# Optimization experiments

Measured on AMD Instinct MI355X. Metric: run time of the kernel, lower is better.

## Reference

```python
import jax, jax.numpy as jnp
import numpy as np

GROUPS = 8
NUM_HEADS = 4
EPS = 1e-5

def setup_inputs() -> dict:
    key = jax.random.key(0)
    k1, k2, k3 = jax.random.split(key, 3)
    B, C, H, W = 4, 128, 64, 64
    x = jax.random.normal(k1, (B, C, H, W), dtype=jnp.float32)
    gn_w = jnp.ones((C,), jnp.float32)
    gn_b = jnp.zeros((C,), jnp.float32)
    qkv_w = jax.random.normal(k2, (3 * C, C), dtype=jnp.float32) * (1.0 / np.sqrt(C))
    qkv_b = jnp.zeros((3 * C,), jnp.float32)
    proj_w = jax.random.normal(k3, (C, C), dtype=jnp.float32) * (1.0 / np.sqrt(C))
    proj_b = jnp.zeros((C,), jnp.float32)
    return {"x": x, "gn_w": gn_w, "gn_b": gn_b, "qkv_w": qkv_w,
            "qkv_b": qkv_b, "proj_w": proj_w, "proj_b": proj_b}

def group_norm(x, w, b):
    B, C, H, W = x.shape
    xg = x.reshape(B, GROUPS, C // GROUPS, H, W)
    mean = jnp.mean(xg, axis=(2, 3, 4), keepdims=True)
    var = jnp.var(xg, axis=(2, 3, 4), keepdims=True)
    xn = ((xg - mean) * jax.lax.rsqrt(var + EPS)).reshape(B, C, H, W)
    return xn * w[None, :, None, None] + b[None, :, None, None]

def reference(x, gn_w, gn_b, qkv_w, qkv_b, proj_w, proj_b):
    B, C, H, W = x.shape
    nh = NUM_HEADS
    hd = C // nh
    xn = group_norm(x, gn_w, gn_b)  # residual is the NORMALIZED x (torch code reassigns x)
    # 1x1 conv == channel matmul
    qkv = jnp.einsum('oc,bchw->bohw', qkv_w, xn) + qkv_b[None, :, None, None]
    qkv = qkv.reshape(B, 3, nh, hd, H * W)
    q, k, v = qkv[:, 0], qkv[:, 1], qkv[:, 2]          # [B, nh, hd, HW]
    attn = jnp.einsum('bhcd,bhce->bhde', q, k) * (C ** -0.5)  # note: full-C scale, as in torch code
    attn = jax.nn.softmax(attn, axis=-1)
    out = jnp.einsum('bhde,bhce->bhcd', attn, v).reshape(B, C, H, W)
    out = jnp.einsum('oc,bchw->bohw', proj_w, out) + proj_b[None, :, None, None]
    return out + xn
```

## Files before the change

### kernel.cpp

```cpp
#include <hip/hip_runtime.h>
#include <math.h>

#define BATCH 4
#define C 128
#define HW 4096
#define G 8
#define CPG 16
#define NH 4
#define HD 32
#define EPS 1e-5f
#define SCALE 0.08838834764831845f
#define LOG2E 1.44269504088896340f
#define KP 40
#define GP 136

typedef unsigned int uint;
typedef unsigned short ushort;
typedef __attribute__((ext_vector_type(8))) short bf16x8;
typedef __attribute__((ext_vector_type(4))) float f32x4;

__device__ __forceinline__ ushort f2bf(float x) {
  uint u = __float_as_uint(x);
  u += 0x7fff + ((u >> 16) & 1);
  return (ushort)(u >> 16);
}
__device__ __forceinline__ ushort f2bf_r(float x) {
  return (ushort)((__float_as_uint(x) + 0x8000u) >> 16);
}
__device__ __forceinline__ float bf2f(ushort h) {
  return __uint_as_float(((uint)h) << 16);
}
__device__ __forceinline__ uint pk(float a, float b) {
#if __has_builtin(__builtin_amdgcn_cvt_pk_bf16_f32)
  auto r = __builtin_amdgcn_cvt_pk_bf16_f32(a, b);
  union { decltype(r) v; uint u; } x;
  x.v = r;
  return x.u;
#else
  uint ua = __float_as_uint(a) + 0x8000u;
  uint ub = __float_as_uint(b) + 0x8000u;
  return __builtin_amdgcn_perm(ub, ua, 0x07060302);
#endif
}
__device__ __forceinline__ bf16x8 as_bf(uint4 u) {
  union { uint4 a; bf16x8 b; } x; x.a = u; return x.b;
}
__device__ __forceinline__ float fexp2(float x) {
#if __has_builtin(__builtin_amdgcn_exp2f)
  return __builtin_amdgcn_exp2f(x);
#else
  return __exp2f(x);
#endif
}

__global__ __launch_bounds__(256) void gn_part(
    const float* __restrict__ x, float* __restrict__ stats) {
  const int bg = blockIdx.x >> 3, chunk = blockIdx.x & 7;
  const float* xp = x + (size_t)bg * (CPG * HW) + chunk * 8192;
  const int tid = threadIdx.x;
  float s = 0.f, ss = 0.f;
  #pragma unroll
  for (int j = 0; j < 8; j++) {
    float4 v = ((const float4*)xp)[j * 256 + tid];
    s += (v.x + v.y) + (v.z + v.w);
    ss += (v.x * v.x + v.y * v.y) + (v.z * v.z + v.w * v.w);
  }
  #pragma unroll
  for (int off = 32; off; off >>= 1) {
    s  += __shfl_down(s, off);
    ss += __shfl_down(ss, off);
  }
  __shared__ float rs[4], rss[4];
  const int lane = tid & 63, wid = tid >> 6;
  if (lane == 0) { rs[wid] = s; rss[wid] = ss; }
  __syncthreads();
  if (tid == 0) {
    stats[(bg * 8 + chunk) * 2]     = (rs[0] + rs[1]) + (rs[2] + rs[3]);
    stats[(bg * 8 + chunk) * 2 + 1] = (rss[0] + rss[1]) + (rss[2] + rss[3]);
  }
}

__device__ __forceinline__ void gn_coeff(
    const float* __restrict__ stats, const float* __restrict__ w,
    const float* __restrict__ b, int batch, int c, float& ca, float& cb) {
  const int bg = batch * G + (c >> 4);
  float s = 0.f, ss = 0.f;
  #pragma unroll
  for (int k = 0; k < 8; k++) {
    s  += stats[(bg * 8 + k) * 2];
    ss += stats[(bg * 8 + k) * 2 + 1];
  }
  const float mean = s * (1.0f / 65536.0f);
  const float var  = ss * (1.0f / 65536.0f) - mean * mean;
  const float inv  = rsqrtf(var + EPS);
  ca = w[c] * inv;
  cb = b[c] - mean * ca;
}

__global__ __launch_bounds__(256) void qkv_gemm(
    const float* __restrict__ x, const float* __restrict__ stats,
    const float* __restrict__ gnw, const float* __restrict__ gnb,
    const float* __restrict__ w, const float* __restrict__ bias,
    ushort* __restrict__ qkvb) {
  const int b = blockIdx.z, m0 = blockIdx.y * 64, n0 = blockIdx.x * 64;
  const int tid = threadIdx.x, lane = tid & 63, wv = tid >> 6;
  const int li = lane & 15, g = lane >> 4;
  __shared__ ushort Ws[64][GP];
  __shared__ ushort Xs[64][GP];
  __shared__ float CA[C], CB[C];

  if (tid < C) gn_coeff(stats, gnw, gnb, b, tid, CA[tid], CB[tid]);
  __syncthreads();

  {
    const int row = tid >> 2, c0 = (tid & 3) * 32;
    const float* wr = w + (size_t)(m0 + row) * C + c0;
    #pragma unroll
    for (int k = 0; k < 4; k++) {
      float4 f0 = ((const float4*)wr)[k * 2];
      float4 f1 = ((const float4*)wr)[k * 2 + 1];
      uint4 u = {pk(f0.x, f0.y), pk(f0.z, f0.w), pk(f1.x, f1.y), pk(f1.z, f1.w)};
      *(uint4*)&Ws[row][c0 + k * 8] = u;
    }
  }
  {
    const int nX = tid & 63, c0 = (tid >> 6) * 32;
    const float* xb = x + (size_t)(b * C + c0) * HW + n0 + nX;
    #pragma unroll
    for (int k = 0; k < 4; k++) {
      float xv[8];
      #pragma unroll
      for (int j = 0; j < 8; j++) {
        int c = c0 + k * 8 + j;
        xv[j] = fmaf(xb[(size_t)(k * 8 + j) * HW], CA[c], CB[c]);
      }
      uint4 u = {pk(xv[0], xv[1]), pk(xv[2], xv[3]), pk(xv[4], xv[5]), pk(xv[6], xv[7])};
      *(uint4*)&Xs[nX][c0 + k * 8] = u;
    }
  }
  __syncthreads();

  f32x4 acc[4];
  #pragma unroll
  for (int nt = 0; nt < 4; nt++) acc[nt] = (f32x4){0.f, 0.f, 0.f, 0.f};
  #pragma unroll
  for (int kk = 0; kk < 4; kk++) {
    bf16x8 af = *(const bf16x8*)&Ws[wv * 16 + li][kk * 32 + g * 8];
    #pragma unroll
    for (int nt = 0; nt < 4; nt++) {
      bf16x8 bfr = *(const bf16x8*)&Xs[nt * 16 + li][kk * 32 + g * 8];
      acc[nt] = __builtin_amdgcn_mfma_f32_16x16x32_bf16(af, bfr, acc[nt], 0, 0, 0);
    }
  }
  const int ob = m0 + wv * 16 + g * 4;
  #pragma unroll
  for (int r = 0; r < 4; r++) {
    float bi = bias[ob + r];
    #pragma unroll
    for (int nt = 0; nt < 4; nt++) {
      qkvb[(size_t)(b * 3 * C + ob + r) * HW + n0 + nt * 16 + li] = f2bf(acc[nt][r] + bi);
    }
  }
}

__global__ __launch_bounds__(256) void kvprep_kernel(
    const ushort* __restrict__ qkvb, ushort* __restrict__ kt) {
  const int bh = blockIdx.y, b = bh >> 2, h = bh & 3;
  const int e0 = blockIdx.x * 64;
  const ushort* kp = qkvb + (size_t)(b * 3 * C + C + h * HD) * HW;
  ushort* ktp = kt + (size_t)bh * HW * HD;
  const int t = threadIdx.x;

  __shared__ ushort Kt[32][66];
  {
    const int c = t >> 3, e8 = (t & 7) * 8;
    *(uint4*)&Kt[c][e8] = *(const uint4*)&kp[(size_t)c * HW + e0 + e8];
  }
  __syncthreads();
  {
    const int e = t >> 2, c0 = (t & 3) * 8;
    ushort o[8];
    #pragma unroll
    for (int j = 0; j < 8; j++) o[j] = Kt[c0 + j][e];
    uint4 u;
    u.x = o[0] | ((uint)o[1] << 16);
    u.y = o[2] | ((uint)o[3] << 16);
    u.z = o[4] | ((uint)o[5] << 16);
    u.w = o[6] | ((uint)o[7] << 16);
    *(uint4*)&ktp[(size_t)(e0 + e) * HD + c0] = u;
  }
}

__global__ __launch_bounds__(512, 4) void attn_kernel(
    ushort* __restrict__ qkv, const ushort* __restrict__ kt) {
  const int bh = blockIdx.y, b = bh >> 2, h = bh & 3;
  const int tid = threadIdx.x, lane = tid & 63, wv = tid >> 6;
  const int li = lane & 15, g = lane >> 4;
  const int grp = wv >> 2, w4 = wv & 3;
  ushort* qp = qkv + (size_t)(b * 3 * C + h * HD) * HW;
  const ushort* vpl = qkv + (size_t)(b * 3 * C + 2 * C + h * HD) * HW;
  const ushort* ktp = kt + (size_t)bh * HW * HD;
  const int d0 = blockIdx.x * 128 + w4 * 32;

  struct SmemT {
    union {
      struct { ushort Ks[2][2][32][KP]; ushort Vs[2][2][32][KP]; } t;
      float OP[8][64][19];
    };
  };
  __shared__ SmemT sm;

  const float qs = SCALE * LOG2E;
  bf16x8 qf[2];
  #pragma unroll
  for (int dt = 0; dt < 2; dt++) {
    int d = d0 + dt * 16 + li;
    float qv[8];
    #pragma unroll
    for (int j = 0; j < 8; j++)
      qv[j] = bf2f(qp[(size_t)(g * 8 + j) * HW + d]) * qs;
    uint4 qu = {pk(qv[0], qv[1]), pk(qv[2], qv[3]), pk(qv[4], qv[5]), pk(qv[6], qv[7])};
    qf[dt] = as_bf(qu);
  }

  f32x4 O[2][2];
  #pragma unroll
  for (int dt = 0; dt < 2; dt++)
    #pragma unroll
    for (int ct = 0; ct < 2; ct++) O[dt][ct] = (f32x4){0.f, 0.f, 0.f, 0.f};
  f32x4 lacc[2] = {(f32x4){0.f, 0.f, 0.f, 0.f}, (f32x4){0.f, 0.f, 0.f, 0.f}};
  const uint one2 = 0x3F803F80u;
  const bf16x8 ones = as_bf((uint4){one2, one2, one2, one2});

  const int gt = tid & 255;
  const bool isK = gt < 128;
  const int t2 = gt & 127;
  const int srow = t2 >> 2, scol8 = (t2 & 3) * 8;
  const ushort* gK = ktp + (size_t)(grp * 64) * 1024 + t2 * 8;
  const ushort* gV = vpl + (size_t)srow * HW + grp * 2048 + scol8;

  uint4 st = isK ? *(const uint4*)&gK[0] : *(const uint4*)&gV[0];
  if (isK) *(uint4*)&sm.t.Ks[grp][0][srow][scol8] = st;
  else     *(uint4*)&sm.t.Vs[grp][0][srow][scol8] = st;
  st = isK ? *(const uint4*)&gK[1024] : *(const uint4*)&gV[32];
  __syncthreads();

  for (int it = 0; it < 64; it++) {
    const int cur = it & 1, nxt = cur ^ 1;
    if (isK) *(uint4*)&sm.t.Ks[grp][nxt][srow][scol8] = st;
    else     *(uint4*)&sm.t.Vs[grp][nxt][srow][scol8] = st;

    bf16x8 kf0 = *(const bf16x8*)&sm.t.Ks[grp][cur][li][g * 8];
    bf16x8 kf1 = *(const bf16x8*)&sm.t.Ks[grp][cur][16 + li][g * 8];
    uint2 va0 = *(const uint2*)&sm.t.Vs[grp][cur][li][4 * g];
    uint2 va1 = *(const uint2*)&sm.t.Vs[grp][cur][li][16 + 4 * g];
    uint2 vb0 = *(const uint2*)&sm.t.Vs[grp][cur][16 + li][4 * g];
    uint2 vb1 = *(const uint2*)&sm.t.Vs[grp][cur][16 + li][16 + 4 * g];
    bf16x8 vf0 = as_bf((uint4){va0.x, va0.y, va1.x, va1.y});
    bf16x8 vf1 = as_bf((uint4){vb0.x, vb0.y, vb1.x, vb1.y});

    const int tn = (it + 2) & 63;
    st = isK ? *(const uint4*)&gK[(size_t)tn * 1024] : *(const uint4*)&gV[tn * 32];

    const f32x4 z = (f32x4){0.f, 0.f, 0.f, 0.f};
    #pragma unroll
    for (int dt = 0; dt < 2; dt++) {
      f32x4 s0 = __builtin_amdgcn_mfma_f32_16x16x32_bf16(kf0, qf[dt], z, 0, 0, 0);
      f32x4 s1 = __builtin_amdgcn_mfma_f32_16x16x32_bf16(kf1, qf[dt], z, 0, 0, 0);
      float p0 = fexp2(s0[0]), p1 = fexp2(s0[1]), p2 = fexp2(s0[2]), p3 = fexp2(s0[3]);
      float p4 = fexp2(s1[0]), p5 = fexp2(s1[1]), p6 = fexp2(s1[2]), p7 = fexp2(s1[3]);
      uint4 pu = {pk(p0, p1), pk(p2, p3), pk(p4, p5), pk(p6, p7)};
      bf16x8 pf = as_bf(pu);
      lacc[dt] = __builtin_amdgcn_mfma_f32_16x16x32_bf16(ones, pf, lacc[dt], 0, 0, 0);
      O[dt][0] = __builtin_amdgcn_mfma_f32_16x16x32_bf16(vf0, pf, O[dt][0], 0, 0, 0);
      O[dt][1] = __builtin_amdgcn_mfma_f32_16x16x32_bf16(vf1, pf, O[dt][1], 0, 0, 0);
    }
    __syncthreads();
  }

  #pragma unroll
  for (int dt = 0; dt < 2; dt++) {
    #pragma unroll
    for (int ct = 0; ct < 2; ct++)
      #pragma unroll
      for (int r = 0; r < 4; r++) sm.OP[wv][lane][dt * 8 + ct * 4 + r] = O[dt][ct][r];
    sm.OP[wv][lane][16 + dt] = lacc[dt][0];
  }
  __syncthreads();
  const int pw = wv ^ 4;
  #pragma unroll
  for (int dt = 0; dt < 2; dt++) {
    const float inv = 1.0f / (lacc[dt][0] + sm.OP[pw][lane][16 + dt]);
    const int d = d0 + dt * 16 + li;
    #pragma unroll
    for (int r = 0; r < 4; r++) {
      float val = O[dt][grp][r] + sm.OP[pw][lane][dt * 8 + grp * 4 + r];
      qp[(size_t)(grp * 16 + g * 4 + r) * HW + d] = f2bf_r(val * inv);
    }
  }
}

__global__ __launch_bounds__(256) void proj_gemm(
    const ushort* __restrict__ qkvb, const float* __restrict__ w,
    const float* __restrict__ bias, const float* __restrict__ x,
    const float* __restrict__ stats, const float* __restrict__ gnw,
    const float* __restrict__ gnb, float* __restrict__ out) {
  const int b = blockIdx.z, m0 = blockIdx.y * 64, n0 = blockIdx.x * 64;
  const int tid = threadIdx.x, lane = tid & 63, wv = tid >> 6;
  const int li = lane & 15, g = lane >> 4;
  __shared__ ushort Ws[64][GP];
  __shared__ ushort Xs[64][GP];
  __shared__ float CA[64], CB[64];

  if (tid < 64) gn_coeff(stats, gnw, gnb, b, m0 + tid, CA[tid], CB[tid]);

  {
    const int row = tid >> 2, c0 = (tid & 3) * 32;
    const float* wr = w + (size_t)(m0 + row) * C + c0;
    #pragma unroll
    for (int k = 0; k < 4; k++) {
      float4 f0 = ((const float4*)wr)[k * 2];
      float4 f1 = ((const float4*)wr)[k * 2 + 1];
      uint4 u = {pk(f0.x, f0.y), pk(f0.z, f0.w), pk(f1.x, f1.y), pk(f1.z, f1.w)};
      *(uint4*)&Ws[row][c0 + k * 8] = u;
    }
  }
  {
    const int nX = tid & 63, c0 = (tid >> 6) * 32;
    const ushort* xb = qkvb + (size_t)(b * 3 * C + c0) * HW + n0 + nX;
    #pragma unroll
    for (int k = 0; k < 4; k++) {
      ushort t8[8];
      #pragma unroll
      for (int j = 0; j < 8; j++) t8[j] = xb[(size_t)(k * 8 + j) * HW];
      uint4 u;
      u.x = t8[0] | ((uint)t8[1] << 16);
      u.y = t8[2] | ((uint)t8[3] << 16);
      u.z = t8[4] | ((uint)t8[5] << 16);
      u.w = t8[6] | ((uint)t8[7] << 16);
      *(uint4*)&Xs[nX][c0 + k * 8] = u;
    }
  }
  __syncthreads();

  f32x4 acc[4];
  #pragma unroll
  for (int nt = 0; nt < 4; nt++) acc[nt] = (f32x4){0.f, 0.f, 0.f, 0.f};
  #pragma unroll
  for (int kk = 0; kk < 4; kk++) {
    bf16x8 af = *(const bf16x8*)&Ws[wv * 16 + li][kk * 32 + g * 8];
    #pragma unroll
    for (int nt = 0; nt < 4; nt++) {
      bf16x8 bfr = *(const bf16x8*)&Xs[nt * 16 + li][kk * 32 + g * 8];
      acc[nt] = __builtin_amdgcn_mfma_f32_16x16x32_bf16(af, bfr, acc[nt], 0, 0, 0);
    }
  }
  const int ob = m0 + wv * 16 + g * 4;
  #pragma unroll
  for (int r = 0; r < 4; r++) {
    const float bi = bias[ob + r];
    const float ca = CA[wv * 16 + g * 4 + r], cb = CB[wv * 16 + g * 4 + r];
    #pragma unroll
    for (int nt = 0; nt < 4; nt++) {
      size_t idx = (size_t)(b * C + ob + r) * HW + n0 + nt * 16 + li;
      out[idx] = acc[nt][r] + bi + fmaf(x[idx], ca, cb);
    }
  }
}

extern "C" void kernel_launch(void* const* d_in, const int* in_sizes, int n_in,
                              void* d_out, int out_size, void* d_ws, size_t ws_size,
                              hipStream_t stream) {
  const float* x     = (const float*)d_in[0];
  const float* gn_w  = (const float*)d_in[1];
  const float* gn_b  = (const float*)d_in[2];
  const float* qkv_w = (const float*)d_in[3];
  const float* qkv_b = (const float*)d_in[4];
  const float* pw    = (const float*)d_in[5];
  const float* pb    = (const float*)d_in[6];
  float* out = (float*)d_out;

  float*  stats = (float*)d_ws;
  ushort* qkvb  = (ushort*)((char*)d_ws + 4096);
  ushort* kt    = qkvb + (size_t)BATCH * 3 * C * HW;

  gn_part<<<dim3(256), dim3(256), 0, stream>>>(x, stats);
  qkv_gemm<<<dim3(HW / 64, 6, BATCH), dim3(256), 0, stream>>>(
      x, stats, gn_w, gn_b, qkv_w, qkv_b, qkvb);
  kvprep_kernel<<<dim3(HW / 64, BATCH * NH), dim3(256), 0, stream>>>(qkvb, kt);
  attn_kernel<<<dim3(HW / 128, BATCH * NH), dim3(512), 0, stream>>>(qkvb, kt);
  proj_gemm<<<dim3(HW / 64, 2, BATCH), dim3(256), 0, stream>>>(
      qkvb, pw, pb, x, stats, gn_w, gn_b, out);
}
```

Measured before the change: 162.1 us.

## Fuse K transpose into QKV GEMM epilogue and drop kvprep kernel

The QKV GEMM now writes the K block straight into the transposed [e][HD] layout used by attention, so the separate kvprep transpose kernel and its extra read/write pass over K are gone. The attention kernel's shared-memory union of K/V tiles and the output-reduction buffer is also split into separate arrays. The K epilogue now does scattered 2-byte stores with a stride of HD, which coalesces poorly. The attention kernel's larger shared-memory footprint (~59KB vs ~39KB) may reduce occupancy under launch_bounds(512,4).

```diff
diff --git a/kernel.cpp b/kernel.cpp
--- a/kernel.cpp
+++ b/kernel.cpp
@@ -11,7 +11,6 @@
 #define EPS 1e-5f
 #define SCALE 0.08838834764831845f
 #define LOG2E 1.44269504088896340f
-#define KP 40
 #define GP 136
 
 typedef unsigned int uint;
@@ -101,7 +100,7 @@
     const float* __restrict__ x, const float* __restrict__ stats,
     const float* __restrict__ gnw, const float* __restrict__ gnb,
     const float* __restrict__ w, const float* __restrict__ bias,
-    ushort* __restrict__ qkvb) {
+    ushort* __restrict__ qkvb, ushort* __restrict__ kt) {
   const int b = blockIdx.z, m0 = blockIdx.y * 64, n0 = blockIdx.x * 64;
   const int tid = threadIdx.x, lane = tid & 63, wv = tid >> 6;
   const int li = lane & 15, g = lane >> 4;
@@ -153,41 +152,29 @@
     }
   }
   const int ob = m0 + wv * 16 + g * 4;
-  #pragma unroll
-  for (int r = 0; r < 4; r++) {
-    float bi = bias[ob + r];
-    #pragma unroll
-    for (int nt = 0; nt < 4; nt++) {
-      qkvb[(size_t)(b * 3 * C + ob + r) * HW + n0 + nt * 16 + li] = f2bf(acc[nt][r] + bi);
-    }
-  }
-}
-
-__global__ __launch_bounds__(256) void kvprep_kernel(
-    const ushort* __restrict__ qkvb, ushort* __restrict__ kt) {
-  const int bh = blockIdx.y, b = bh >> 2, h = bh & 3;
-  const int e0 = blockIdx.x * 64;
-  const ushort* kp = qkvb + (size_t)(b * 3 * C + C + h * HD) * HW;
-  ushort* ktp = kt + (size_t)bh * HW * HD;
-  const int t = threadIdx.x;
-
-  __shared__ ushort Kt[32][66];
-  {
-    const int c = t >> 3, e8 = (t & 7) * 8;
-    *(uint4*)&Kt[c][e8] = *(const uint4*)&kp[(size_t)c * HW + e0 + e8];
-  }
-  __syncthreads();
-  {
-    const int e = t >> 2, c0 = (t & 3) * 8;
-    ushort o[8];
-    #pragma unroll
-    for (int j = 0; j < 8; j++) o[j] = Kt[c0 + j][e];
-    uint4 u;
-    u.x = o[0] | ((uint)o[1] << 16);
-    u.y = o[2] | ((uint)o[3] << 16);
-    u.z = o[4] | ((uint)o[5] << 16);
-    u.w = o[6] | ((uint)o[7] << 16);
-    *(uint4*)&ktp[(size_t)(e0 + e) * HD + c0] = u;
+  if (blockIdx.y == 2 || blockIdx.y == 3) {
+    const int ck = ob - C;
+    const int h  = ck >> 5;
+    const int cl = ck & 31;
+    ushort* ktp = kt + (size_t)(b * NH + h) * HW * HD;
+    #pragma unroll
+    for (int r = 0; r < 4; r++) {
+      float bi = bias[ob + r];
+      #pragma unroll
+      for (int nt = 0; nt < 4; nt++) {
+        int e = n0 + nt * 16 + li;
+        ktp[(size_t)e * HD + cl + r] = f2bf(acc[nt][r] + bi);
+      }
+    }
+  } else {
+    #pragma unroll
+    for (int r = 0; r < 4; r++) {
+      float bi = bias[ob + r];
+      #pragma unroll
+      for (int nt = 0; nt < 4; nt++) {
+        qkvb[(size_t)(b * 3 * C + ob + r) * HW + n0 + nt * 16 + li] = f2bf(acc[nt][r] + bi);
+      }
+    }
   }
 }
 
@@ -202,13 +189,9 @@
   const ushort* ktp = kt + (size_t)bh * HW * HD;
   const int d0 = blockIdx.x * 128 + w4 * 32;
 
-  struct SmemT {
-    union {
-      struct { ushort Ks[2][2][32][KP]; ushort Vs[2][2][32][KP]; } t;
-      float OP[8][64][19];
-    };
-  };
-  __shared__ SmemT sm;
+  __shared__ ushort Ks[2][2][32][40];
+  __shared__ ushort Vs[2][2][32][40];
+  __shared__ float OP[8][64][19];
 
   const float qs = SCALE * LOG2E;
   bf16x8 qf[2];
@@ -240,22 +223,22 @@
   const ushort* gV = vpl + (size_t)srow * HW + grp * 2048 + scol8;
 
   uint4 st = isK ? *(const uint4*)&gK[0] : *(const uint4*)&gV[0];
-  if (isK) *(uint4*)&sm.t.Ks[grp][0][srow][scol8] = st;
-  else     *(uint4*)&sm.t.Vs[grp][0][srow][scol8] = st;
+  if (isK) *(uint4*)&Ks[grp][0][srow][scol8] = st;
+  else     *(uint4*)&Vs[grp][0][srow][scol8] = st;
   st = isK ? *(const uint4*)&gK[1024] : *(const uint4*)&gV[32];
   __syncthreads();
 
   for (int it = 0; it < 64; it++) {
     const int cur = it & 1, nxt = cur ^ 1;
-    if (isK) *(uint4*)&sm.t.Ks[grp][nxt][srow][scol8] = st;
-    else     *(uint4*)&sm.t.Vs[grp][nxt][srow][scol8] = st;
-
-    bf16x8 kf0 = *(const bf16x8*)&sm.t.Ks[grp][cur][li][g * 8];
-    bf16x8 kf1 = *(const bf16x8*)&sm.t.Ks[grp][cur][16 + li][g * 8];
-    uint2 va0 = *(const uint2*)&sm.t.Vs[grp][cur][li][4 * g];
-    uint2 va1 = *(const uint2*)&sm.t.Vs[grp][cur][li][16 + 4 * g];
-    uint2 vb0 = *(const uint2*)&sm.t.Vs[grp][cur][16 + li][4 * g];
-    uint2 vb1 = *(const uint2*)&sm.t.Vs[grp][cur][16 + li][16 + 4 * g];
+    if (isK) *(uint4*)&Ks[grp][nxt][srow][scol8] = st;
+    else     *(uint4*)&Vs[grp][nxt][srow][scol8] = st;
+
+    bf16x8 kf0 = *(const bf16x8*)&Ks[grp][cur][li][g * 8];
+    bf16x8 kf1 = *(const bf16x8*)&Ks[grp][cur][16 + li][g * 8];
+    uint2 va0 = *(const uint2*)&Vs[grp][cur][li][4 * g];
+    uint2 va1 = *(const uint2*)&Vs[grp][cur][li][16 + 4 * g];
+    uint2 vb0 = *(const uint2*)&Vs[grp][cur][16 + li][4 * g];
+    uint2 vb1 = *(const uint2*)&Vs[grp][cur][16 + li][16 + 4 * g];
     bf16x8 vf0 = as_bf((uint4){va0.x, va0.y, va1.x, va1.y});
     bf16x8 vf1 = as_bf((uint4){vb0.x, vb0.y, vb1.x, vb1.y});
 
@@ -283,18 +266,18 @@
     #pragma unroll
     for (int ct = 0; ct < 2; ct++)
       #pragma unroll
-      for (int r = 0; r < 4; r++) sm.OP[wv][lane][dt * 8 + ct * 4 + r] = O[dt][ct][r];
-    sm.OP[wv][lane][16 + dt] = lacc[dt][0];
+      for (int r = 0; r < 4; r++) OP[wv][lane][dt * 8 + ct * 4 + r] = O[dt][ct][r];
+    OP[wv][lane][16 + dt] = lacc[dt][0];
   }
   __syncthreads();
   const int pw = wv ^ 4;
   #pragma unroll
   for (int dt = 0; dt < 2; dt++) {
-    const float inv = 1.0f / (lacc[dt][0] + sm.OP[pw][lane][16 + dt]);
+    const float inv = 1.0f / (lacc[dt][0] + OP[pw][lane][16 + dt]);
     const int d = d0 + dt * 16 + li;
     #pragma unroll
     for (int r = 0; r < 4; r++) {
-      float val = O[dt][grp][r] + sm.OP[pw][lane][dt * 8 + grp * 4 + r];
+      float val = O[dt][grp][r] + OP[pw][lane][dt * 8 + grp * 4 + r];
       qp[(size_t)(grp * 16 + g * 4 + r) * HW + d] = f2bf_r(val * inv);
     }
   }
@@ -386,8 +369,7 @@
 
   gn_part<<<dim3(256), dim3(256), 0, stream>>>(x, stats);
   qkv_gemm<<<dim3(HW / 64, 6, BATCH), dim3(256), 0, stream>>>(
-      x, stats, gn_w, gn_b, qkv_w, qkv_b, qkvb);
-  kvprep_kernel<<<dim3(HW / 64, BATCH * NH), dim3(256), 0, stream>>>(qkvb, kt);
+      x, stats, gn_w, gn_b, qkv_w, qkv_b, qkvb, kt);
   attn_kernel<<<dim3(HW / 128, BATCH * NH), dim3(512), 0, stream>>>(qkvb, kt);
   proj_gemm<<<dim3(HW / 64, 2, BATCH), dim3(256), 0, stream>>>(
       qkvb, pw, pb, x, stats, gn_w, gn_b, out);
```

Measured after the change: 144.4 us. 1.12x faster.
